# Performance work log

Hardware: AMD Instinct MI355X
Metric: run time of the kernel (lower is better)

## Reference

```python
import jax, jax.numpy as jnp
import numpy as np

BN_EPS = 1e-5


def setup_inputs() -> dict:
    key = jax.random.key(0)
    k1, k2, k3 = jax.random.split(key, 3)
    C = 192
    inputs = jax.random.normal(k1, (32, C, 112, 112), dtype=jnp.float32)
    # Depthwise kernels: one 3x3 filter per channel -> OIHW with I=1, groups=C
    w = jax.random.normal(k2, (C, 1, 3, 3), dtype=jnp.float32) * 0.1
    b = jax.random.normal(k3, (C,), dtype=jnp.float32) * 0.1
    gamma = jnp.ones((C,), dtype=jnp.float32)
    beta = jnp.zeros((C,), dtype=jnp.float32)
    return {"inputs": inputs, "w": w, "b": b, "gamma": gamma, "beta": beta}


def reference(inputs, w, b, gamma, beta):
    C = w.shape[0]
    stride = 1
    # Depthwise 3x3 conv (equivalent to the per-channel Conv2d loop + concat)
    y = jax.lax.conv_general_dilated(
        inputs, w,
        window_strides=(stride, stride),
        padding=((1, 1), (1, 1)),
        dimension_numbers=("NCHW", "OIHW", "NCHW"),
        feature_group_count=C,
    ) + b[None, :, None, None]
    # BatchNorm2d in training mode: batch statistics over (N, H, W), biased var
    mean = jnp.mean(y, axis=(0, 2, 3), keepdims=True)
    var = jnp.mean(jnp.square(y - mean), axis=(0, 2, 3), keepdims=True)
    y_hat = (y - mean) * jax.lax.rsqrt(var + BN_EPS)
    z = gamma[None, :, None, None] * y_hat + beta[None, :, None, None]
    # ReLU6
    return jnp.clip(z, 0.0, 6.0)
```

## Files before the change

kernel.cpp:

```cpp
#include <hip/hip_runtime.h>

#define C_   192
#define N_   32
#define H_   112
#define W_   112
#define W4   28
#define PIX  (H_ * W4)
#define BLK  256
#define GX   ((PIX + BLK - 1) / BLK)

__global__ void zero_acc_kernel(float* __restrict__ acc) {
    for (int i = threadIdx.x; i < 2 * C_; i += blockDim.x) acc[i] = 0.0f;
}

__device__ __forceinline__ void conv_row(const float* __restrict__ row, int j,
                                         float w0, float w1, float w2,
                                         float4& acc) {
    const float4 m = *(const float4*)(row + 4 * j);
    const float l = (j > 0)       ? row[4 * j - 1] : 0.0f;
    const float r = (j < W4 - 1)  ? row[4 * j + 4] : 0.0f;
    acc.x += w0 * l   + w1 * m.x + w2 * m.y;
    acc.y += w0 * m.x + w1 * m.y + w2 * m.z;
    acc.z += w0 * m.y + w1 * m.z + w2 * m.w;
    acc.w += w0 * m.z + w1 * m.w + w2 * r;
}

__device__ __forceinline__ float4 conv4(const float* __restrict__ plane,
                                        int h, int j, const float* wc) {
    float4 acc = {0.f, 0.f, 0.f, 0.f};
    if (h > 0)      conv_row(plane + (size_t)(h - 1) * W_, j, wc[0], wc[1], wc[2], acc);
                    conv_row(plane + (size_t)h       * W_, j, wc[3], wc[4], wc[5], acc);
    if (h < H_ - 1) conv_row(plane + (size_t)(h + 1) * W_, j, wc[6], wc[7], wc[8], acc);
    return acc;
}

__global__ __launch_bounds__(BLK) void stats_kernel(const float* __restrict__ in,
                                                    const float* __restrict__ w,
                                                    float* __restrict__ acc) {
    const int nc = blockIdx.y;
    const int c  = nc % C_;
    const int p  = blockIdx.x * BLK + threadIdx.x;

    float wc[9];
#pragma unroll
    for (int k = 0; k < 9; ++k) wc[k] = w[c * 9 + k];

    float s = 0.0f, ss = 0.0f;
    if (p < PIX) {
        const int h = p / W4, j = p % W4;
        const float* plane = in + (size_t)nc * (H_ * W_);
        const float4 y = conv4(plane, h, j, wc);
        s  = (y.x + y.y) + (y.z + y.w);
        ss = (y.x * y.x + y.y * y.y) + (y.z * y.z + y.w * y.w);
    }

#pragma unroll
    for (int off = 32; off > 0; off >>= 1) {
        s  += __shfl_down(s,  off, 64);
        ss += __shfl_down(ss, off, 64);
    }
    __shared__ float ls[BLK / 64], lss[BLK / 64];
    const int lane = threadIdx.x & 63;
    const int wv   = threadIdx.x >> 6;
    if (lane == 0) { ls[wv] = s; lss[wv] = ss; }
    __syncthreads();
    if (threadIdx.x == 0) {
        float S  = 0.f, SS = 0.f;
#pragma unroll
        for (int i = 0; i < BLK / 64; ++i) { S += ls[i]; SS += lss[i]; }
        atomicAdd(&acc[c],      S);
        atomicAdd(&acc[C_ + c], SS);
    }
}

__global__ void finalize_kernel(const float* __restrict__ acc,
                                const float* __restrict__ gamma,
                                const float* __restrict__ beta,
                                float* __restrict__ st) {
    const int c = threadIdx.x;
    if (c < C_) {
        const float M    = (float)N_ * (float)H_ * (float)W_;
        const float mean = acc[c] / M;
        float var        = acc[C_ + c] / M - mean * mean;
        var              = fmaxf(var, 0.0f);
        const float sc   = gamma[c] * rsqrtf(var + 1e-5f);
        st[c]       = sc;
        st[C_ + c]  = beta[c] - sc * mean;
    }
}

__global__ __launch_bounds__(BLK) void apply_kernel(const float* __restrict__ in,
                                                    const float* __restrict__ w,
                                                    const float* __restrict__ st,
                                                    float* __restrict__ out) {
    const int nc = blockIdx.y;
    const int c  = nc % C_;
    const int p  = blockIdx.x * BLK + threadIdx.x;
    if (p >= PIX) return;

    float wc[9];
#pragma unroll
    for (int k = 0; k < 9; ++k) wc[k] = w[c * 9 + k];
    const float sc = st[c];
    const float sh = st[C_ + c];

    const int h = p / W4, j = p % W4;
    const float* plane = in + (size_t)nc * (H_ * W_);
    const float4 y = conv4(plane, h, j, wc);

    float4 z;
    z.x = fminf(fmaxf(sc * y.x + sh, 0.0f), 6.0f);
    z.y = fminf(fmaxf(sc * y.y + sh, 0.0f), 6.0f);
    z.z = fminf(fmaxf(sc * y.z + sh, 0.0f), 6.0f);
    z.w = fminf(fmaxf(sc * y.w + sh, 0.0f), 6.0f);

    *(float4*)(out + (size_t)nc * (H_ * W_) + (size_t)p * 4) = z;
}

extern "C" void kernel_launch(void* const* d_in, const int* in_sizes, int n_in,
                              void* d_out, int out_size, void* d_ws, size_t ws_size,
                              hipStream_t stream) {
    const float* in    = (const float*)d_in[0];
    const float* w     = (const float*)d_in[1];
    const float* gamma = (const float*)d_in[3];
    const float* beta  = (const float*)d_in[4];
    float* out = (float*)d_out;

    float* acc = (float*)d_ws;
    float* st  = acc + 2 * C_;

    hipLaunchKernelGGL(zero_acc_kernel, dim3(1), dim3(64), 0, stream, acc);

    const dim3 grid(GX, N_ * C_);
    hipLaunchKernelGGL(stats_kernel, grid, dim3(BLK), 0, stream, in, w, acc);
    hipLaunchKernelGGL(finalize_kernel, dim3(1), dim3(C_), 0, stream,
                       acc, gamma, beta, st);
    hipLaunchKernelGGL(apply_kernel, grid, dim3(BLK), 0, stream, in, w, st, out);
}
```

Before: 686.7 us.

## Fuse stats and apply into one cooperative kernel with grid sync and reverse plane order

Replaces the four-kernel pipeline (zero, stats, finalize, apply) with a single cooperative kernel. Each of 1024 persistent blocks handles six planes, computes partial sums, then grid-syncs and recomputes the conv in reverse plane order to apply BN and ReLU6. The reverse order is meant to reuse planes still held in the MI355X last-level cache, and output stores are nontemporal. The risks are grid-sync cost, reduced parallelism per plane, and the requirement that all 1024 blocks be co-resident.

```diff
diff --git a/kernel.cpp b/kernel.cpp
--- a/kernel.cpp
+++ b/kernel.cpp
@@ -1,28 +1,32 @@
 #include <hip/hip_runtime.h>
+#include <hip/hip_cooperative_groups.h>
 
-#define C_   192
-#define N_   32
-#define H_   112
-#define W_   112
-#define W4   28
-#define PIX  (H_ * W4)
-#define BLK  256
-#define GX   ((PIX + BLK - 1) / BLK)
+namespace cg = cooperative_groups;
 
-__global__ void zero_acc_kernel(float* __restrict__ acc) {
-    for (int i = threadIdx.x; i < 2 * C_; i += blockDim.x) acc[i] = 0.0f;
-}
+#define C_    192
+#define N_    32
+#define H_    112
+#define W_    112
+#define HW    (H_ * W_)
+#define W4    28
+#define PIX   (H_ * W4)
+#define TPB   256
+#define NBLK  1024
+#define PLANES (N_ * C_)
+#define PPB   (PLANES / NBLK)
+
+typedef float nat4 __attribute__((ext_vector_type(4)));
 
 __device__ __forceinline__ void conv_row(const float* __restrict__ row, int j,
                                          float w0, float w1, float w2,
                                          float4& acc) {
     const float4 m = *(const float4*)(row + 4 * j);
-    const float l = (j > 0)       ? row[4 * j - 1] : 0.0f;
-    const float r = (j < W4 - 1)  ? row[4 * j + 4] : 0.0f;
-    acc.x += w0 * l   + w1 * m.x + w2 * m.y;
-    acc.y += w0 * m.x + w1 * m.y + w2 * m.z;
-    acc.z += w0 * m.y + w1 * m.z + w2 * m.w;
-    acc.w += w0 * m.z + w1 * m.w + w2 * r;
+    const float l = (j > 0)      ? row[4 * j - 1] : 0.0f;
+    const float r = (j < W4 - 1) ? row[4 * j + 4] : 0.0f;
+    acc.x = fmaf(w0, l,   fmaf(w1, m.x, fmaf(w2, m.y, acc.x)));
+    acc.y = fmaf(w0, m.x, fmaf(w1, m.y, fmaf(w2, m.z, acc.y)));
+    acc.z = fmaf(w0, m.y, fmaf(w1, m.z, fmaf(w2, m.w, acc.z)));
+    acc.w = fmaf(w0, m.z, fmaf(w1, m.w, fmaf(w2, r,   acc.w)));
 }
 
 __device__ __forceinline__ float4 conv4(const float* __restrict__ plane,
@@ -34,87 +38,80 @@
     return acc;
 }
 
-__global__ __launch_bounds__(BLK) void stats_kernel(const float* __restrict__ in,
-                                                    const float* __restrict__ w,
-                                                    float* __restrict__ acc) {
-    const int nc = blockIdx.y;
-    const int c  = nc % C_;
-    const int p  = blockIdx.x * BLK + threadIdx.x;
+__global__ __launch_bounds__(TPB, 4) void fused_kernel(
+        const float* __restrict__ in,
+        const float* __restrict__ w,
+        const float* __restrict__ gamma,
+        const float* __restrict__ beta,
+        float* __restrict__ out,
+        float* __restrict__ acc) {
+    cg::grid_group grid = cg::this_grid();
+    const int tid = threadIdx.x;
+    const int bid = blockIdx.x;
 
-    float wc[9];
+    if (bid == 0)
+        for (int i = tid; i < 2 * C_; i += TPB) acc[i] = 0.0f;
+    grid.sync();
+
+    __shared__ float ls[TPB / 64], lss[TPB / 64];
+
+    for (int pl = bid * PPB; pl < bid * PPB + PPB; ++pl) {
+        const int c = pl >> 5, n = pl & 31;
+        const float* plane = in + (size_t)(n * C_ + c) * HW;
+        float wc[9];
 #pragma unroll
-    for (int k = 0; k < 9; ++k) wc[k] = w[c * 9 + k];
+        for (int k = 0; k < 9; ++k) wc[k] = w[c * 9 + k];
 
-    float s = 0.0f, ss = 0.0f;
-    if (p < PIX) {
-        const int h = p / W4, j = p % W4;
-        const float* plane = in + (size_t)nc * (H_ * W_);
-        const float4 y = conv4(plane, h, j, wc);
-        s  = (y.x + y.y) + (y.z + y.w);
-        ss = (y.x * y.x + y.y * y.y) + (y.z * y.z + y.w * y.w);
+        float s = 0.0f, ss = 0.0f;
+        for (int p = tid; p < PIX; p += TPB) {
+            const int h = p / W4, j = p - h * W4;
+            const float4 y = conv4(plane, h, j, wc);
+            s  += (y.x + y.y) + (y.z + y.w);
+            ss += (y.x * y.x + y.y * y.y) + (y.z * y.z + y.w * y.w);
+        }
+#pragma unroll
+        for (int off = 32; off > 0; off >>= 1) {
+            s  += __shfl_down(s,  off, 64);
+            ss += __shfl_down(ss, off, 64);
+        }
+        if ((tid & 63) == 0) { ls[tid >> 6] = s; lss[tid >> 6] = ss; }
+        __syncthreads();
+        if (tid == 0) {
+            const float S  = (ls[0]  + ls[1])  + (ls[2]  + ls[3]);
+            const float SS = (lss[0] + lss[1]) + (lss[2] + lss[3]);
+            atomicAdd(&acc[c],      S);
+            atomicAdd(&acc[C_ + c], SS);
+        }
+        __syncthreads();
     }
 
+    grid.sync();
+
+    for (int pl = bid * PPB + PPB - 1; pl >= bid * PPB; --pl) {
+        const int c = pl >> 5, n = pl & 31;
+        const float* plane  = in  + (size_t)(n * C_ + c) * HW;
+        float*       oplane = out + (size_t)(n * C_ + c) * HW;
+        float wc[9];
 #pragma unroll
-    for (int off = 32; off > 0; off >>= 1) {
-        s  += __shfl_down(s,  off, 64);
-        ss += __shfl_down(ss, off, 64);
+        for (int k = 0; k < 9; ++k) wc[k] = w[c * 9 + k];
+
+        const float M    = (float)N_ * (float)HW;
+        const float mean = acc[c] / M;
+        const float var  = fmaxf(acc[C_ + c] / M - mean * mean, 0.0f);
+        const float sc   = gamma[c] * rsqrtf(var + 1e-5f);
+        const float sh   = beta[c] - sc * mean;
+
+        for (int p = tid; p < PIX; p += TPB) {
+            const int h = p / W4, j = p - h * W4;
+            const float4 y = conv4(plane, h, j, wc);
+            nat4 z;
+            z.x = fminf(fmaxf(fmaf(sc, y.x, sh), 0.0f), 6.0f);
+            z.y = fminf(fmaxf(fmaf(sc, y.y, sh), 0.0f), 6.0f);
+            z.z = fminf(fmaxf(fmaf(sc, y.z, sh), 0.0f), 6.0f);
+            z.w = fminf(fmaxf(fmaf(sc, y.w, sh), 0.0f), 6.0f);
+            __builtin_nontemporal_store(z, (nat4*)(oplane + 4 * p));
+        }
     }
-    __shared__ float ls[BLK / 64], lss[BLK / 64];
-    const int lane = threadIdx.x & 63;
-    const int wv   = threadIdx.x >> 6;
-    if (lane == 0) { ls[wv] = s; lss[wv] = ss; }
-    __syncthreads();
-    if (threadIdx.x == 0) {
-        float S  = 0.f, SS = 0.f;
-#pragma unroll
-        for (int i = 0; i < BLK / 64; ++i) { S += ls[i]; SS += lss[i]; }
-        atomicAdd(&acc[c],      S);
-        atomicAdd(&acc[C_ + c], SS);
-    }
-}
-
-__global__ void finalize_kernel(const float* __restrict__ acc,
-                                const float* __restrict__ gamma,
-                                const float* __restrict__ beta,
-                                float* __restrict__ st) {
-    const int c = threadIdx.x;
-    if (c < C_) {
-        const float M    = (float)N_ * (float)H_ * (float)W_;
-        const float mean = acc[c] / M;
-        float var        = acc[C_ + c] / M - mean * mean;
-        var              = fmaxf(var, 0.0f);
-        const float sc   = gamma[c] * rsqrtf(var + 1e-5f);
-        st[c]       = sc;
-        st[C_ + c]  = beta[c] - sc * mean;
-    }
-}
-
-__global__ __launch_bounds__(BLK) void apply_kernel(const float* __restrict__ in,
-                                                    const float* __restrict__ w,
-                                                    const float* __restrict__ st,
-                                                    float* __restrict__ out) {
-    const int nc = blockIdx.y;
-    const int c  = nc % C_;
-    const int p  = blockIdx.x * BLK + threadIdx.x;
-    if (p >= PIX) return;
-
-    float wc[9];
-#pragma unroll
-    for (int k = 0; k < 9; ++k) wc[k] = w[c * 9 + k];
-    const float sc = st[c];
-    const float sh = st[C_ + c];
-
-    const int h = p / W4, j = p % W4;
-    const float* plane = in + (size_t)nc * (H_ * W_);
-    const float4 y = conv4(plane, h, j, wc);
-
-    float4 z;
-    z.x = fminf(fmaxf(sc * y.x + sh, 0.0f), 6.0f);
-    z.y = fminf(fmaxf(sc * y.y + sh, 0.0f), 6.0f);
-    z.z = fminf(fmaxf(sc * y.z + sh, 0.0f), 6.0f);
-    z.w = fminf(fmaxf(sc * y.w + sh, 0.0f), 6.0f);
-
-    *(float4*)(out + (size_t)nc * (H_ * W_) + (size_t)p * 4) = z;
 }
 
 extern "C" void kernel_launch(void* const* d_in, const int* in_sizes, int n_in,
@@ -125,15 +122,10 @@
     const float* gamma = (const float*)d_in[3];
     const float* beta  = (const float*)d_in[4];
     float* out = (float*)d_out;
+    float* acc = (float*)d_ws;
 
-    float* acc = (float*)d_ws;
-    float* st  = acc + 2 * C_;
-
-    hipLaunchKernelGGL(zero_acc_kernel, dim3(1), dim3(64), 0, stream, acc);
-
-    const dim3 grid(GX, N_ * C_);
-    hipLaunchKernelGGL(stats_kernel, grid, dim3(BLK), 0, stream, in, w, acc);
-    hipLaunchKernelGGL(finalize_kernel, dim3(1), dim3(C_), 0, stream,
-                       acc, gamma, beta, st);
-    hipLaunchKernelGGL(apply_kernel, grid, dim3(BLK), 0, stream, in, w, st, out);
+    void* args[] = {(void*)&in, (void*)&w, (void*)&gamma, (void*)&beta,
+                    (void*)&out, (void*)&acc};
+    hipLaunchCooperativeKernel((void*)fused_kernel, dim3(NBLK), dim3(TPB),
+                               args, 0, stream);
 }
```

Result: slower. 899.4 us (+31.0%).
